# Optimization experiments

Hardware: AMD Instinct MI355X
Metric: run time of the kernel (lower is better)

Reference implementation:

```python
import jax, jax.numpy as jnp
import numpy as np

B, C, N = 8, 256, 4096

def setup_inputs() -> dict:
    key = jax.random.key(0)
    k1, k2, k3 = jax.random.split(key, 3)
    pts_feat = jax.random.normal(k1, (B, C, N), dtype=jnp.float32)
    # Conv1d(channels, channels, 1, bias=False) weight is [C_out, C_in, 1] -> store as [C_out, C_in]
    scale = 1.0 / np.sqrt(C)
    Wq = jax.random.uniform(k2, (C, C), dtype=jnp.float32, minval=-scale, maxval=scale)
    Wk = jax.random.uniform(k3, (C, C), dtype=jnp.float32, minval=-scale, maxval=scale)
    return {"pts_feat": pts_feat, "Wq": Wq, "Wk": Wk}

def reference(pts_feat, Wq, Wk):
    # 1x1 conv == channel-wise matmul. x_q: [B, N, C], x_k: [B, C, N]
    x_q = jnp.einsum('bcn,dc->bnd', pts_feat, Wq)
    x_k = jnp.einsum('bcn,dc->bdn', pts_feat, Wk)
    logits = jnp.einsum('bnc,bcm->bnm', x_q, x_k)          # [B, N, N]
    attn = jax.nn.softmax(logits, axis=-1)
    attn = attn / (1e-8 + attn.sum(axis=-1, keepdims=True))
    # torch.einsum('bnn,bnc->bnc', attn, feat) takes the DIAGONAL of attn
    # and scales each point's raw feature vector by it (no contraction).
    diag = jnp.diagonal(attn, axis1=1, axis2=2)            # [B, N]
    x_attn = pts_feat * diag[:, None, :]                   # [B, C, N]
    return x_attn
```

## Files before the change

kernel.cpp:

```cpp
#include <hip/hip_runtime.h>
#include <hip/hip_bf16.h>
#include <cstdint>

#define B_ 8
#define C_ 256
#define N_ 4096

typedef __bf16 bf16;
typedef __bf16 bf16x8 __attribute__((ext_vector_type(8)));
typedef float f32x4 __attribute__((ext_vector_type(4)));
typedef unsigned int u32;

__device__ __forceinline__ void async_ld16(const void* g, void* l) {
  __builtin_amdgcn_global_load_lds(
      (const __attribute__((address_space(1))) void*)g,
      (__attribute__((address_space(3))) void*)l, 16, 0, 0);
}

__device__ __forceinline__ float bh2f(unsigned short u) {
  union { u32 i; float f; } x; x.i = ((u32)u) << 16; return x.f;
}
__device__ __forceinline__ unsigned short f2bh(float f) {
  union { float f; u32 i; } x; x.f = f;
  u32 i = x.i + 0x7fffu + ((x.i >> 16) & 1u);
  return (unsigned short)(i >> 16);
}

__device__ __forceinline__ bool wave_sniff_fp32(const unsigned short* p) {
  int l = threadIdx.x & 63;
  unsigned short u = p[2 * l];
  int e = (u >> 7) & 0xff;
  unsigned long long m = __ballot(e >= 112 && e <= 142);
  return __popcll(m) < 32;
}

__global__ __launch_bounds__(256) void k_mt(const void* __restrict__ Wqv,
                                            const void* __restrict__ Wkv,
                                            unsigned short* __restrict__ Mt) {
  bool fq = wave_sniff_fp32((const unsigned short*)Wqv);
  bool fk = wave_sniff_fp32((const unsigned short*)Wkv);
  __shared__ float wkcol[C_];
  int d = blockIdx.x;
  int c = threadIdx.x;
  if (fk)
    wkcol[c] = ((const float*)Wkv)[c * C_ + d];
  else
    wkcol[c] = bh2f(((const unsigned short*)Wkv)[c * C_ + d]);
  __syncthreads();
  float acc = 0.f;
  if (fq) {
    for (int e0 = 0; e0 < C_; e0 += 16) {
      float wq[16];
#pragma unroll
      for (int j = 0; j < 16; ++j) wq[j] = ((const float*)Wqv)[(e0 + j) * C_ + c];
#pragma unroll
      for (int j = 0; j < 16; ++j) acc += wkcol[e0 + j] * wq[j];
    }
  } else {
    for (int e0 = 0; e0 < C_; e0 += 16) {
      float wq[16];
#pragma unroll
      for (int j = 0; j < 16; ++j) wq[j] = bh2f(((const unsigned short*)Wqv)[(e0 + j) * C_ + c]);
#pragma unroll
      for (int j = 0; j < 16; ++j) acc += wkcol[e0 + j] * wq[j];
    }
  }
  Mt[(size_t)d * C_ + c] = f2bh(acc);
}

__global__ __launch_bounds__(256) void k_transpose(const void* __restrict__ Fv,
                                                   unsigned short* __restrict__ Ft) {
  bool f32 = wave_sniff_fp32((const unsigned short*)Fv);
  __shared__ unsigned short tile[64 * 66];
  int n0 = blockIdx.x * 64, c0 = blockIdx.y * 64, b = blockIdx.z;
  int t = threadIdx.x;
#pragma unroll
  for (int p = 0; p < 2; ++p) {
    int c = (t >> 3) + 32 * p;
    int n = (t & 7) * 8;
    size_t off = (size_t)(b * C_ + c0 + c) * N_ + n0 + n;
    unsigned short vals[8];
    if (f32) {
      const float* src = (const float*)Fv + off;
      float4 v0 = *(const float4*)(src);
      float4 v1 = *(const float4*)(src + 4);
      vals[0] = f2bh(v0.x); vals[1] = f2bh(v0.y); vals[2] = f2bh(v0.z); vals[3] = f2bh(v0.w);
      vals[4] = f2bh(v1.x); vals[5] = f2bh(v1.y); vals[6] = f2bh(v1.z); vals[7] = f2bh(v1.w);
    } else {
      uint4 v = *(const uint4*)((const unsigned short*)Fv + off);
      vals[0] = (unsigned short)(v.x & 0xffffu); vals[1] = (unsigned short)(v.x >> 16);
      vals[2] = (unsigned short)(v.y & 0xffffu); vals[3] = (unsigned short)(v.y >> 16);
      vals[4] = (unsigned short)(v.z & 0xffffu); vals[5] = (unsigned short)(v.z >> 16);
      vals[6] = (unsigned short)(v.w & 0xffffu); vals[7] = (unsigned short)(v.w >> 16);
    }
#pragma unroll
    for (int s = 0; s < 8; ++s) tile[c * 66 + n + s] = vals[s];
  }
  __syncthreads();
#pragma unroll
  for (int p = 0; p < 4; ++p) {
    int n = (t >> 4) + 16 * p;
    int cq = (t & 15) * 4;
    unsigned short e0 = tile[(cq + 0) * 66 + n];
    unsigned short e1 = tile[(cq + 1) * 66 + n];
    unsigned short e2 = tile[(cq + 2) * 66 + n];
    unsigned short e3 = tile[(cq + 3) * 66 + n];
    uint2 o;
    o.x = ((u32)e1 << 16) | e0;
    o.y = ((u32)e3 << 16) | e2;
    *(uint2*)(Ft + ((size_t)(b * N_ + n0 + n) * C_ + c0 + cq)) = o;
  }
}

__global__ __launch_bounds__(256, 2) void k_proj(const bf16* __restrict__ Ft,
                                                 const bf16* __restrict__ Mt,
                                                 bf16* __restrict__ G) {
  __shared__ bf16 As[8 * 128 * 32];
  int n0 = blockIdx.x * 128;
  int b = blockIdx.y;
  int d0 = blockIdx.z * 128;
  int t = threadIdx.x, w = t >> 6, l = t & 63;
  int lr = l & 15, lq = l >> 4;
  int wn = w * 32;
  const size_t fbase = (size_t)b * N_ * C_;

  int schunk = ((t & 3) ^ ((t >> 3) & 3)) * 8;
#pragma unroll
  for (int kc = 0; kc < 8; ++kc)
#pragma unroll
    for (int r = 0; r < 2; ++r)
      async_ld16(Ft + fbase + (size_t)(n0 + r * 64 + (t >> 2)) * C_ + kc * 32 + schunk,
                 As + kc * 4096 + (r * 256 + t) * 8);

  bf16x8 bb[2][8];
#pragma unroll
  for (int j = 0; j < 2; ++j)
#pragma unroll
    for (int kc = 0; kc < 8; ++kc)
      bb[j][kc] = *(const bf16x8*)(Mt + (size_t)(d0 + wn + 16 * j + lr) * C_ + kc * 32 + lq * 8);

  __syncthreads();
  int rchunk = (lq ^ ((lr >> 1) & 3)) * 8;
  f32x4 acc[8][2] = {};
#pragma unroll
  for (int kc = 0; kc < 8; ++kc) {
#pragma unroll
    for (int i = 0; i < 8; ++i) {
      bf16x8 a = *(const bf16x8*)(As + kc * 4096 + (16 * i + lr) * 32 + rchunk);
#pragma unroll
      for (int j = 0; j < 2; ++j)
        acc[i][j] = __builtin_amdgcn_mfma_f32_16x16x32_bf16(a, bb[j][kc], acc[i][j], 0, 0, 0);
    }
  }
#pragma unroll
  for (int i = 0; i < 8; ++i)
#pragma unroll
    for (int j = 0; j < 2; ++j)
#pragma unroll
      for (int r = 0; r < 4; ++r) {
        int row = n0 + 16 * i + lq * 4 + r;
        int col = d0 + wn + 16 * j + lr;
        G[fbase + (size_t)row * C_ + col] = (bf16)acc[i][j][r];
      }
}

__global__ __launch_bounds__(256, 4) void k_attn(const bf16* __restrict__ G,
                                                 const bf16* __restrict__ Ft,
                                                 float* __restrict__ snn,
                                                 float* __restrict__ lsum) {
  __shared__ bf16 Ks[8 * 64 * 32];
  int bid = blockIdx.x;
  int b = bid & 7, q = (bid >> 3) & 3, ntile = bid >> 5;
  int n0 = ntile * 128;
  int t = threadIdx.x, w = t >> 6, l = t & 63;
  int lr = l & 15, lq = l >> 4;
  int wrow = w * 32;
  const size_t gbase = (size_t)b * N_ * C_;

  bf16x8 a[2][8];
#pragma unroll
  for (int i = 0; i < 2; ++i)
#pragma unroll
    for (int kc = 0; kc < 8; ++kc)
      a[i][kc] = *(const bf16x8*)(G + gbase + (size_t)(n0 + wrow + 16 * i + lr) * C_ + kc * 32 + lq * 8);

  float part[8];
#pragma unroll
  for (int s = 0; s < 8; ++s) part[s] = 0.f;

  int m_base = q * 1024;
  bool has_diag = (q == (ntile >> 3));
  int d0 = (ntile & 7) * 2;

  int srow = t >> 2;
  int schunk = ((t & 3) ^ ((t >> 3) & 3)) * 8;
  int rchunk = (lq ^ ((lr >> 1) & 3)) * 8;

  for (int it = 0; it < 16; ++it) {
    int m0 = m_base + it * 64;
    __syncthreads();
#pragma unroll
    for (int kc = 0; kc < 8; ++kc)
      async_ld16(Ft + gbase + (size_t)(m0 + srow) * C_ + kc * 32 + schunk,
                 Ks + kc * 2048 + t * 8);
    __syncthreads();
    f32x4 acc[2][4] = {};
#pragma unroll
    for (int kc = 0; kc < 8; ++kc) {
      bf16x8 bb[4];
#pragma unroll
      for (int j = 0; j < 4; ++j)
        bb[j] = *(const bf16x8*)(Ks + kc * 2048 + (16 * j + lr) * 32 + rchunk);
#pragma unroll
      for (int i = 0; i < 2; ++i)
#pragma unroll
        for (int j = 0; j < 4; ++j)
          acc[i][j] = __builtin_amdgcn_mfma_f32_16x16x32_bf16(a[i][kc], bb[j], acc[i][j], 0, 0, 0);
    }
    bool dit = has_diag && ((it >> 1) == (ntile & 7));
#pragma unroll
    for (int i = 0; i < 2; ++i)
#pragma unroll
      for (int j = 0; j < 4; ++j)
#pragma unroll
        for (int r = 0; r < 4; ++r) {
          float e = __expf(acc[i][j][r]);
          part[i * 4 + r] += e;
          if (dit) {
            int rloc = wrow + 16 * i + lq * 4 + r;
            int cloc = 16 * j + lr;
            if ((it - d0) * 64 + cloc == rloc) snn[b * N_ + n0 + rloc] = e;
          }
        }
  }

#pragma unroll
  for (int s = 0; s < 8; ++s) {
    float v = part[s];
    v += __shfl_xor(v, 1);
    v += __shfl_xor(v, 2);
    v += __shfl_xor(v, 4);
    v += __shfl_xor(v, 8);
    part[s] = v;
  }
  if (lr == 0) {
#pragma unroll
    for (int i = 0; i < 2; ++i)
#pragma unroll
      for (int r = 0; r < 4; ++r)
        lsum[((size_t)q * B_ + b) * N_ + n0 + wrow + 16 * i + lq * 4 + r] = part[i * 4 + r];
  }
}

__global__ __launch_bounds__(256) void k_scale(const void* __restrict__ Fv,
                                               const float* __restrict__ snn,
                                               const float* __restrict__ lsum,
                                               void* __restrict__ Outv) {
  bool f32 = wave_sniff_fp32((const unsigned short*)Fv);
  int g = blockIdx.x * 256 + threadIdx.x;
  size_t base = (size_t)g * 8;
  int n = (int)(base & (N_ - 1));
  int b = (int)(base >> 20);
  float4 s0 = *(const float4*)(snn + (size_t)b * N_ + n);
  float4 s1 = *(const float4*)(snn + (size_t)b * N_ + n + 4);
  float ls[8];
#pragma unroll
  for (int k = 0; k < 8; ++k) ls[k] = 0.f;
#pragma unroll
  for (int p = 0; p < 4; ++p) {
    float4 l0 = *(const float4*)(lsum + ((size_t)p * B_ + b) * N_ + n);
    float4 l1 = *(const float4*)(lsum + ((size_t)p * B_ + b) * N_ + n + 4);
    ls[0] += l0.x; ls[1] += l0.y; ls[2] += l0.z; ls[3] += l0.w;
    ls[4] += l1.x; ls[5] += l1.y; ls[6] += l1.z; ls[7] += l1.w;
  }
  const float c1 = 1.0f + 1e-8f;
  float dd[8];
  dd[0] = s0.x / (ls[0] * c1); dd[1] = s0.y / (ls[1] * c1);
  dd[2] = s0.z / (ls[2] * c1); dd[3] = s0.w / (ls[3] * c1);
  dd[4] = s1.x / (ls[4] * c1); dd[5] = s1.y / (ls[5] * c1);
  dd[6] = s1.z / (ls[6] * c1); dd[7] = s1.w / (ls[7] * c1);
  if (f32) {
    const float* F = (const float*)Fv + base;
    float* O = (float*)Outv + base;
    float4 a0 = *(const float4*)(F);
    float4 a1 = *(const float4*)(F + 4);
    float4 o0, o1;
    o0.x = a0.x * dd[0]; o0.y = a0.y * dd[1]; o0.z = a0.z * dd[2]; o0.w = a0.w * dd[3];
    o1.x = a1.x * dd[4]; o1.y = a1.y * dd[5]; o1.z = a1.z * dd[6]; o1.w = a1.w * dd[7];
    *(float4*)(O) = o0;
    *(float4*)(O + 4) = o1;
  } else {
    uint4 v = *(const uint4*)((const unsigned short*)Fv + base);
    u32 vv[4] = {v.x, v.y, v.z, v.w};
    u32 o[4];
#pragma unroll
    for (int k = 0; k < 4; ++k) {
      float lo = bh2f((unsigned short)(vv[k] & 0xffffu)) * dd[2 * k];
      float hi = bh2f((unsigned short)(vv[k] >> 16)) * dd[2 * k + 1];
      o[k] = ((u32)f2bh(hi) << 16) | f2bh(lo);
    }
    uint4 ov; ov.x = o[0]; ov.y = o[1]; ov.z = o[2]; ov.w = o[3];
    *(uint4*)((unsigned short*)Outv + base) = ov;
  }
}

extern "C" void kernel_launch(void* const* d_in, const int* in_sizes, int n_in,
                              void* d_out, int out_size, void* d_ws, size_t ws_size,
                              hipStream_t stream) {
  (void)in_sizes; (void)n_in; (void)out_size; (void)ws_size;
  const void* F = d_in[0];
  const void* Wq = d_in[1];
  const void* Wk = d_in[2];
  char* ws = (char*)d_ws;
  bf16* Ft = (bf16*)(ws);
  bf16* G = (bf16*)(ws + (16u << 20));
  char* tail = ws + (32u << 20);
  float* snn = (float*)(tail);
  float* lsum = (float*)(tail + 131072);
  bf16* Mt = (bf16*)(tail + 131072 + 524288);

  k_mt<<<256, 256, 0, stream>>>(Wq, Wk, (unsigned short*)Mt);
  k_transpose<<<dim3(N_ / 64, C_ / 64, B_), 256, 0, stream>>>(F, (unsigned short*)Ft);
  k_proj<<<dim3(N_ / 128, B_, 2), 256, 0, stream>>>(Ft, Mt, G);
  k_attn<<<1024, 256, 0, stream>>>(G, Ft, snn, lsum);
  k_scale<<<(B_ * C_ * N_ / 8) / 256, 256, 0, stream>>>(F, snn, lsum, d_out);
}
```

Baseline: 187.1 us.

## Switch attention kernel to 32x32x16 MFMA and merge weight/transpose prep kernels

Rewrites the logits/exp-sum kernel to use the 32x32x16 bf16 MFMA with a 32-column K tile, which changes the LDS swizzle, per-lane register layout and diagonal extraction. The key range is split into 8 quarters instead of 4, doubling the grid, so k_scale now sums 8 partial row sums and the workspace offset for Mt moves to make room. The Mt weight product and the feature transpose are merged into a single launch, removing one kernel launch. The intent is fewer MFMA issues per FLOP and more parallel blocks. The cost is smaller tiles that need more synchronisation per unit of work, plus extra partial-sum traffic.

```diff
diff --git a/kernel.cpp b/kernel.cpp
--- a/kernel.cpp
+++ b/kernel.cpp
@@ -9,6 +9,7 @@
 typedef __bf16 bf16;
 typedef __bf16 bf16x8 __attribute__((ext_vector_type(8)));
 typedef float f32x4 __attribute__((ext_vector_type(4)));
+typedef float f32x16 __attribute__((ext_vector_type(16)));
 typedef unsigned int u32;
 
 __device__ __forceinline__ void async_ld16(const void* g, void* l) {
@@ -34,46 +35,48 @@
   return __popcll(m) < 32;
 }
 
-__global__ __launch_bounds__(256) void k_mt(const void* __restrict__ Wqv,
-                                            const void* __restrict__ Wkv,
-                                            unsigned short* __restrict__ Mt) {
-  bool fq = wave_sniff_fp32((const unsigned short*)Wqv);
-  bool fk = wave_sniff_fp32((const unsigned short*)Wkv);
+__global__ __launch_bounds__(256) void k_pre(const void* __restrict__ Wqv,
+                                             const void* __restrict__ Wkv,
+                                             const void* __restrict__ Fv,
+                                             unsigned short* __restrict__ Mt,
+                                             unsigned short* __restrict__ Ft) {
   __shared__ float wkcol[C_];
-  int d = blockIdx.x;
-  int c = threadIdx.x;
-  if (fk)
-    wkcol[c] = ((const float*)Wkv)[c * C_ + d];
-  else
-    wkcol[c] = bh2f(((const unsigned short*)Wkv)[c * C_ + d]);
-  __syncthreads();
-  float acc = 0.f;
-  if (fq) {
-    for (int e0 = 0; e0 < C_; e0 += 16) {
-      float wq[16];
-#pragma unroll
-      for (int j = 0; j < 16; ++j) wq[j] = ((const float*)Wqv)[(e0 + j) * C_ + c];
-#pragma unroll
-      for (int j = 0; j < 16; ++j) acc += wkcol[e0 + j] * wq[j];
-    }
-  } else {
-    for (int e0 = 0; e0 < C_; e0 += 16) {
-      float wq[16];
-#pragma unroll
-      for (int j = 0; j < 16; ++j) wq[j] = bh2f(((const unsigned short*)Wqv)[(e0 + j) * C_ + c]);
-#pragma unroll
-      for (int j = 0; j < 16; ++j) acc += wkcol[e0 + j] * wq[j];
-    }
-  }
-  Mt[(size_t)d * C_ + c] = f2bh(acc);
-}
-
-__global__ __launch_bounds__(256) void k_transpose(const void* __restrict__ Fv,
-                                                   unsigned short* __restrict__ Ft) {
+  __shared__ unsigned short tile[64 * 66];
+  int bid = blockIdx.x;
+  int t = threadIdx.x;
+  if (bid < 256) {
+    bool fq = wave_sniff_fp32((const unsigned short*)Wqv);
+    bool fk = wave_sniff_fp32((const unsigned short*)Wkv);
+    int d = bid, c = t;
+    if (fk)
+      wkcol[c] = ((const float*)Wkv)[c * C_ + d];
+    else
+      wkcol[c] = bh2f(((const unsigned short*)Wkv)[c * C_ + d]);
+    __syncthreads();
+    float acc = 0.f;
+    if (fq) {
+      for (int e0 = 0; e0 < C_; e0 += 16) {
+        float wq[16];
+#pragma unroll
+        for (int j = 0; j < 16; ++j) wq[j] = ((const float*)Wqv)[(e0 + j) * C_ + c];
+#pragma unroll
+        for (int j = 0; j < 16; ++j) acc += wkcol[e0 + j] * wq[j];
+      }
+    } else {
+      for (int e0 = 0; e0 < C_; e0 += 16) {
+        float wq[16];
+#pragma unroll
+        for (int j = 0; j < 16; ++j) wq[j] = bh2f(((const unsigned short*)Wqv)[(e0 + j) * C_ + c]);
+#pragma unroll
+        for (int j = 0; j < 16; ++j) acc += wkcol[e0 + j] * wq[j];
+      }
+    }
+    Mt[(size_t)d * C_ + c] = f2bh(acc);
+    return;
+  }
   bool f32 = wave_sniff_fp32((const unsigned short*)Fv);
-  __shared__ unsigned short tile[64 * 66];
-  int n0 = blockIdx.x * 64, c0 = blockIdx.y * 64, b = blockIdx.z;
-  int t = threadIdx.x;
+  int id = bid - 256;
+  int n0 = (id & 63) * 64, c0 = ((id >> 6) & 3) * 64, b = id >> 8;
 #pragma unroll
   for (int p = 0; p < 2; ++p) {
     int c = (t >> 3) + 32 * p;
@@ -168,87 +171,72 @@
                                                  const bf16* __restrict__ Ft,
                                                  float* __restrict__ snn,
                                                  float* __restrict__ lsum) {
-  __shared__ bf16 Ks[8 * 64 * 32];
+  __shared__ bf16 Ks[32 * 256];
   int bid = blockIdx.x;
-  int b = bid & 7, q = (bid >> 3) & 3, ntile = bid >> 5;
+  int b = bid & 7, q = (bid >> 3) & 7, ntile = bid >> 6;
   int n0 = ntile * 128;
   int t = threadIdx.x, w = t >> 6, l = t & 63;
-  int lr = l & 15, lq = l >> 4;
+  int lm = l & 31, hi = l >> 5;
   int wrow = w * 32;
   const size_t gbase = (size_t)b * N_ * C_;
 
-  bf16x8 a[2][8];
-#pragma unroll
-  for (int i = 0; i < 2; ++i)
-#pragma unroll
-    for (int kc = 0; kc < 8; ++kc)
-      a[i][kc] = *(const bf16x8*)(G + gbase + (size_t)(n0 + wrow + 16 * i + lr) * C_ + kc * 32 + lq * 8);
-
-  float part[8];
-#pragma unroll
-  for (int s = 0; s < 8; ++s) part[s] = 0.f;
-
-  int m_base = q * 1024;
-  bool has_diag = (q == (ntile >> 3));
-  int d0 = (ntile & 7) * 2;
-
-  int srow = t >> 2;
-  int schunk = ((t & 3) ^ ((t >> 3) & 3)) * 8;
-  int rchunk = (lq ^ ((lr >> 1) & 3)) * 8;
+  bf16x8 a[16];
+#pragma unroll
+  for (int kc = 0; kc < 16; ++kc)
+    a[kc] = *(const bf16x8*)(G + gbase + (size_t)(n0 + wrow + lm) * C_ + kc * 16 + hi * 8);
+
+  float part[16];
+#pragma unroll
+  for (int s = 0; s < 16; ++s) part[s] = 0.f;
+
+  int m_base = q * 512;
 
   for (int it = 0; it < 16; ++it) {
-    int m0 = m_base + it * 64;
+    int m0 = m_base + it * 32;
     __syncthreads();
 #pragma unroll
-    for (int kc = 0; kc < 8; ++kc)
-      async_ld16(Ft + gbase + (size_t)(m0 + srow) * C_ + kc * 32 + schunk,
-                 Ks + kc * 2048 + t * 8);
+    for (int u = 0; u < 4; ++u) {
+      int s = w * 4 + u;
+      int row = 2 * s + hi;
+      int c = (lm ^ (row & 7)) * 8;
+      async_ld16(Ft + gbase + (size_t)(m0 + row) * C_ + c, Ks + s * 512);
+    }
     __syncthreads();
-    f32x4 acc[2][4] = {};
-#pragma unroll
-    for (int kc = 0; kc < 8; ++kc) {
-      bf16x8 bb[4];
-#pragma unroll
-      for (int j = 0; j < 4; ++j)
-        bb[j] = *(const bf16x8*)(Ks + kc * 2048 + (16 * j + lr) * 32 + rchunk);
-#pragma unroll
-      for (int i = 0; i < 2; ++i)
-#pragma unroll
-        for (int j = 0; j < 4; ++j)
-          acc[i][j] = __builtin_amdgcn_mfma_f32_16x16x32_bf16(a[i][kc], bb[j], acc[i][j], 0, 0, 0);
-    }
-    bool dit = has_diag && ((it >> 1) == (ntile & 7));
-#pragma unroll
-    for (int i = 0; i < 2; ++i)
-#pragma unroll
-      for (int j = 0; j < 4; ++j)
-#pragma unroll
-        for (int r = 0; r < 4; ++r) {
-          float e = __expf(acc[i][j][r]);
-          part[i * 4 + r] += e;
-          if (dit) {
-            int rloc = wrow + 16 * i + lq * 4 + r;
-            int cloc = 16 * j + lr;
-            if ((it - d0) * 64 + cloc == rloc) snn[b * N_ + n0 + rloc] = e;
-          }
-        }
-  }
-
-#pragma unroll
-  for (int s = 0; s < 8; ++s) {
+    f32x16 acc = {};
+#pragma unroll
+    for (int kc = 0; kc < 16; ++kc) {
+      int gp = (kc * 2 + hi) ^ (lm & 7);
+      bf16x8 bb = *(const bf16x8*)(Ks + lm * 256 + gp * 8);
+      acc = __builtin_amdgcn_mfma_f32_32x32x16_bf16(a[kc], bb, acc, 0, 0, 0);
+    }
+    bool dit = (m0 == n0 + wrow);
+#pragma unroll
+    for (int reg = 0; reg < 16; ++reg) {
+      float e = __expf(acc[reg]);
+      part[reg] += e;
+      if (dit) {
+        int rloc = (reg & 3) + 8 * (reg >> 2) + 4 * hi;
+        if (lm == rloc) snn[b * N_ + n0 + wrow + rloc] = e;
+      }
+    }
+  }
+
+#pragma unroll
+  for (int s = 0; s < 16; ++s) {
     float v = part[s];
     v += __shfl_xor(v, 1);
     v += __shfl_xor(v, 2);
     v += __shfl_xor(v, 4);
     v += __shfl_xor(v, 8);
+    v += __shfl_xor(v, 16);
     part[s] = v;
   }
-  if (lr == 0) {
-#pragma unroll
-    for (int i = 0; i < 2; ++i)
-#pragma unroll
-      for (int r = 0; r < 4; ++r)
-        lsum[((size_t)q * B_ + b) * N_ + n0 + wrow + 16 * i + lq * 4 + r] = part[i * 4 + r];
+  if (lm == 0) {
+#pragma unroll
+    for (int reg = 0; reg < 16; ++reg) {
+      int rloc = (reg & 3) + 8 * (reg >> 2) + 4 * hi;
+      lsum[((size_t)q * B_ + b) * N_ + n0 + wrow + rloc] = part[reg];
+    }
   }
 }
 
@@ -267,7 +255,7 @@
 #pragma unroll
   for (int k = 0; k < 8; ++k) ls[k] = 0.f;
 #pragma unroll
-  for (int p = 0; p < 4; ++p) {
+  for (int p = 0; p < 8; ++p) {
     float4 l0 = *(const float4*)(lsum + ((size_t)p * B_ + b) * N_ + n);
     float4 l1 = *(const float4*)(lsum + ((size_t)p * B_ + b) * N_ + n + 4);
     ls[0] += l0.x; ls[1] += l0.y; ls[2] += l0.z; ls[3] += l0.w;
@@ -317,11 +305,10 @@
   char* tail = ws + (32u << 20);
   float* snn = (float*)(tail);
   float* lsum = (float*)(tail + 131072);
-  bf16* Mt = (bf16*)(tail + 131072 + 524288);
-
-  k_mt<<<256, 256, 0, stream>>>(Wq, Wk, (unsigned short*)Mt);
-  k_transpose<<<dim3(N_ / 64, C_ / 64, B_), 256, 0, stream>>>(F, (unsigned short*)Ft);
+  bf16* Mt = (bf16*)(tail + 131072 + 1048576);
+
+  k_pre<<<256 + 2048, 256, 0, stream>>>(Wq, Wk, F, (unsigned short*)Mt, (unsigned short*)Ft);
   k_proj<<<dim3(N_ / 128, B_, 2), 256, 0, stream>>>(Ft, Mt, G);
-  k_attn<<<1024, 256, 0, stream>>>(G, Ft, snn, lsum);
+  k_attn<<<2048, 256, 0, stream>>>(G, Ft, snn, lsum);
   k_scale<<<(B_ * C_ * N_ / 8) / 256, 256, 0, stream>>>(F, snn, lsum, d_out);
 }
```

After: 202.5 us. +8.3%, slower.
